# Optimization experiments

Hardware: AMD Instinct MI355X
Metric: run time of the kernel (lower is better)

## Reference

```python
import jax, jax.numpy as jnp
import numpy as np

# Layer configuration (from init_kwargs)
T = 32
TSEQ = jnp.linspace(1.0 / T, 1.0, T, dtype=jnp.float32)  # tseq grid
N_HOM_DIMS = 2      # dimensions = [0, 1]
KMAX = 4            # KK = [0,1,2,3] -> top-4 landscapes

B, N, P = 128, 256 * 256, 4096  # batch, grid cells, persistence pairs


def setup_inputs() -> dict:
    key = jax.random.key(0)
    k1, k2, k3, k4 = jax.random.split(key, 4)
    fun_value = jax.random.uniform(k1, (B, N), dtype=jnp.float32)
    birth_idx = jax.random.randint(k2, (B, P), 0, N, dtype=jnp.int32)
    death_idx = jax.random.randint(k3, (B, P), 0, N, dtype=jnp.int32)
    pair_dim = jax.random.randint(k4, (B, P), 0, N_HOM_DIMS, dtype=jnp.int32)
    return {"fun_value": fun_value, "birth_idx": birth_idx,
            "death_idx": death_idx, "pair_dim": pair_dim}


def reference(fun_value, birth_idx, death_idx, pair_dim):
    # Gather birth/death filtration values of each persistence pair
    # (this is fun_value[locationBirth] / fun_value[locationDeath]).
    b = jnp.take_along_axis(fun_value, birth_idx, axis=-1)   # [B, P]
    d = jnp.take_along_axis(fun_value, death_idx, axis=-1)   # [B, P]
    # Tent functions: fab[b, t, p] = max(min(tseq[t] - birth_p, death_p - tseq[t]), 0)
    fab = jnp.maximum(
        jnp.minimum(TSEQ[None, :, None] - b[:, None, :],
                    d[:, None, :] - TSEQ[None, :, None]),
        0.0)                                                  # [B, T, P]
    # Restrict pairs to each homology dimension; out-of-dim pairs become the
    # zero padding the original code uses in its fab buffer.
    dims = jnp.arange(N_HOM_DIMS, dtype=pair_dim.dtype)
    in_dim = pair_dim[:, None, None, :] == dims[None, :, None, None]  # [B, D, 1, P]
    fab_d = jnp.where(in_dim, fab[:, None, :, :], 0.0)        # [B, D, T, P]
    # Landscape = top-KMAX values over pairs (== -sort(-fab)[..., KK]).
    land, _ = jax.lax.top_k(fab_d, KMAX)                      # [B, D, T, KMAX]
    return land
```

## Files before the change

### kernel.cpp

```cpp
#include <hip/hip_runtime.h>

#define B_ 128
#define N_ 65536
#define P_ 4096
#define T_ 32
#define D_ 2
#define K_ 4
#define S_ 8
#define PAIRS_PER_BLOCK (P_ / S_)
#define PAIRS_PER_WAVE (PAIRS_PER_BLOCK / 4)

__global__ __launch_bounds__(256) void gather_bd(
        const float* __restrict__ fun,
        const int* __restrict__ bidx,
        const int* __restrict__ didx,
        float2* __restrict__ bd) {
    int tid = blockIdx.x * 256 + threadIdx.x;
    int batch = tid >> 12;
    const float* f = fun + (size_t)batch * N_;
    float b = f[bidx[tid]];
    float d = f[didx[tid]];
    bd[tid] = make_float2(b, d);
}

__global__ __launch_bounds__(256) void scan_top4(
        const float2* __restrict__ bd,
        const int* __restrict__ pdim,
        float* __restrict__ partial) {
    __shared__ float2 bdS[PAIRS_PER_BLOCK];
    __shared__ int    pdS[PAIRS_PER_BLOCK];
    __shared__ float  mrg[4][64][4];

    int batch = blockIdx.x;
    int slice = blockIdx.y;
    int tid   = threadIdx.x;
    int base  = batch * P_ + slice * PAIRS_PER_BLOCK;

    for (int i = tid; i < PAIRS_PER_BLOCK; i += 256) {
        bdS[i] = bd[base + i];
        pdS[i] = pdim[base + i];
    }
    __syncthreads();

    int lane  = tid & 63;
    int wave  = tid >> 6;
    int t     = lane & 31;
    int mydim = lane >> 5;
    float tf  = (float)(t + 1) * 0.03125f;

    float v0 = 0.f, v1 = 0.f, v2 = 0.f, v3 = 0.f;
    int p0 = wave * PAIRS_PER_WAVE;
    #pragma unroll 4
    for (int i = 0; i < PAIRS_PER_WAVE; ++i) {
        float2 bdv = bdS[p0 + i];
        int   pd   = pdS[p0 + i];
        float tv   = fminf(tf - bdv.x, bdv.y - tf);
        float val  = (pd == mydim) ? tv : 0.0f;
        val = fmaxf(val, 0.0f);
        float x;
        x = fminf(v0, val); v0 = fmaxf(v0, val); val = x;
        x = fminf(v1, val); v1 = fmaxf(v1, val); val = x;
        x = fminf(v2, val); v2 = fmaxf(v2, val); val = x;
        v3 = fmaxf(v3, val);
    }

    mrg[wave][lane][0] = v0;
    mrg[wave][lane][1] = v1;
    mrg[wave][lane][2] = v2;
    mrg[wave][lane][3] = v3;
    __syncthreads();

    if (wave == 0) {
        float u0 = 0.f, u1 = 0.f, u2 = 0.f, u3 = 0.f;
        #pragma unroll
        for (int w = 0; w < 4; ++w) {
            #pragma unroll
            for (int k = 0; k < 4; ++k) {
                float val = mrg[w][lane][k];
                float x;
                x = fminf(u0, val); u0 = fmaxf(u0, val); val = x;
                x = fminf(u1, val); u1 = fmaxf(u1, val); val = x;
                x = fminf(u2, val); u2 = fmaxf(u2, val); val = x;
                u3 = fmaxf(u3, val);
            }
        }
        float* dst = partial + (((size_t)batch * S_ + slice) * 64 + lane) * 4;
        dst[0] = u0; dst[1] = u1; dst[2] = u2; dst[3] = u3;
    }
}

__global__ __launch_bounds__(256) void final_merge(
        const float* __restrict__ partial,
        float* __restrict__ out) {
    int tid = blockIdx.x * 256 + threadIdx.x;
    int batch = tid >> 6;
    int combo = tid & 63;
    float u0 = 0.f, u1 = 0.f, u2 = 0.f, u3 = 0.f;
    for (int s = 0; s < S_; ++s) {
        const float* src = partial + (((size_t)batch * S_ + s) * 64 + combo) * 4;
        #pragma unroll
        for (int k = 0; k < 4; ++k) {
            float val = src[k];
            float x;
            x = fminf(u0, val); u0 = fmaxf(u0, val); val = x;
            x = fminf(u1, val); u1 = fmaxf(u1, val); val = x;
            x = fminf(u2, val); u2 = fmaxf(u2, val); val = x;
            u3 = fmaxf(u3, val);
        }
    }
    float* dst = out + (size_t)tid * 4;
    dst[0] = u0; dst[1] = u1; dst[2] = u2; dst[3] = u3;
}

extern "C" void kernel_launch(void* const* d_in, const int* in_sizes, int n_in,
                              void* d_out, int out_size, void* d_ws, size_t ws_size,
                              hipStream_t stream) {
    const float* fun  = (const float*)d_in[0];
    const int*   bidx = (const int*)d_in[1];
    const int*   didx = (const int*)d_in[2];
    const int*   pdim = (const int*)d_in[3];
    float* out = (float*)d_out;

    float2* bdw     = (float2*)d_ws;
    float*  partial = (float*)d_ws + (size_t)B_ * P_ * 2;

    gather_bd<<<(B_ * P_) / 256, 256, 0, stream>>>(fun, bidx, didx, bdw);

    dim3 g2(B_, S_);
    scan_top4<<<g2, 256, 0, stream>>>(bdw, pdim, partial);

    final_merge<<<(B_ * 64) / 256, 256, 0, stream>>>(partial, out);
}
```

Before: 107.4 us.

## Fuse gather into scan, partition pairs by dimension, remap blocks per XCD

Merges the gather and scan kernels so each block reads its filtration values directly into shared memory, with no round trip through a workspace buffer. Within the block, pairs are split by homology dimension using ballot and prefix counts. Each half-wave then handles every pair of one dimension, rather than masking out half of all pairs. Block indices are remapped so that each XCD handles a contiguous group of batches, which should improve L2 locality of the gathered rows. The cost is extra ballot and prefix-sum overhead and uneven loop lengths between waves.

```diff
diff --git a/kernel.cpp b/kernel.cpp
--- a/kernel.cpp
+++ b/kernel.cpp
@@ -7,109 +7,143 @@
 #define D_ 2
 #define K_ 4
 #define S_ 8
-#define PAIRS_PER_BLOCK (P_ / S_)
-#define PAIRS_PER_WAVE (PAIRS_PER_BLOCK / 4)
+#define PPB 512
 
-__global__ __launch_bounds__(256) void gather_bd(
+#define INS(v0, v1, v2, v3, val)                                  \
+    {                                                             \
+        float _x = fminf(v0, val); v0 = fmaxf(v0, val);           \
+        float _y = fminf(v1, _x);  v1 = fmaxf(v1, _x);            \
+        float _z = fminf(v2, _y);  v2 = fmaxf(v2, _y);            \
+        v3 = fmaxf(v3, _z);                                       \
+    }
+
+__global__ __launch_bounds__(256) void fused_scan(
         const float* __restrict__ fun,
         const int* __restrict__ bidx,
         const int* __restrict__ didx,
-        float2* __restrict__ bd) {
-    int tid = blockIdx.x * 256 + threadIdx.x;
-    int batch = tid >> 12;
-    const float* f = fun + (size_t)batch * N_;
-    float b = f[bidx[tid]];
-    float d = f[didx[tid]];
-    bd[tid] = make_float2(b, d);
-}
-
-__global__ __launch_bounds__(256) void scan_top4(
-        const float2* __restrict__ bd,
         const int* __restrict__ pdim,
         float* __restrict__ partial) {
-    __shared__ float2 bdS[PAIRS_PER_BLOCK];
-    __shared__ int    pdS[PAIRS_PER_BLOCK];
+    __shared__ float2 bdS[PPB + 8];
+    __shared__ int    cntS[8];
     __shared__ float  mrg[4][64][4];
 
-    int batch = blockIdx.x;
-    int slice = blockIdx.y;
-    int tid   = threadIdx.x;
-    int base  = batch * P_ + slice * PAIRS_PER_BLOCK;
+    int bid   = blockIdx.x;
+    int xcd   = bid & 7;
+    int seq   = bid >> 3;
+    int batch = xcd * 16 + (seq & 15);
+    int slice = seq >> 4;
 
-    for (int i = tid; i < PAIRS_PER_BLOCK; i += 256) {
-        bdS[i] = bd[base + i];
-        pdS[i] = pdim[base + i];
+    int tid  = threadIdx.x;
+    int lane = tid & 63;
+    int wave = tid >> 6;
+    int base = batch * P_ + slice * PPB;
+
+    const float* f = fun + (size_t)batch * N_;
+    int p0 = base + tid, p1 = base + 256 + tid;
+    int pd0 = pdim[p0], pd1 = pdim[p1];
+    float b0 = f[bidx[p0]], d0 = f[didx[p0]];
+    float b1 = f[bidx[p1]], d1 = f[didx[p1]];
+
+    unsigned long long bal0 = __ballot(pd0 == 0);
+    unsigned long long bal1 = __ballot(pd1 == 0);
+    if (lane == 0) {
+        cntS[wave * 2]     = __popcll(bal0);
+        cntS[wave * 2 + 1] = __popcll(bal1);
     }
     __syncthreads();
 
-    int lane  = tid & 63;
-    int wave  = tid >> 6;
-    int t     = lane & 31;
-    int mydim = lane >> 5;
-    float tf  = (float)(t + 1) * 0.03125f;
+    int s0 = wave * 2, s1 = s0 + 1;
+    int pre0_s0 = 0, pre1_s0 = 0, pre0_s1 = 0, pre1_s1 = 0, n0tot = 0;
+    #pragma unroll
+    for (int s = 0; s < 8; ++s) {
+        int cs = cntS[s];
+        if (s < s0) { pre0_s0 += cs; pre1_s0 += 64 - cs; }
+        if (s < s1) { pre0_s1 += cs; pre1_s1 += 64 - cs; }
+        n0tot += cs;
+    }
+    int n1tot = PPB - n0tot;
+    int A   = (n0tot + 1) & ~1;
+    int n1p = (n1tot + 1) & ~1;
 
-    float v0 = 0.f, v1 = 0.f, v2 = 0.f, v3 = 0.f;
-    int p0 = wave * PAIRS_PER_WAVE;
+    unsigned long long lmask = (1ull << lane) - 1ull;
+    int r0 = __popcll(bal0 & lmask);
+    int r1 = __popcll(bal1 & lmask);
+    int dst0 = (pd0 == 0) ? (pre0_s0 + r0) : (A + pre1_s0 + (lane - r0));
+    int dst1 = (pd1 == 0) ? (pre0_s1 + r1) : (A + pre1_s1 + (lane - r1));
+    bdS[dst0] = make_float2(b0, d0);
+    bdS[dst1] = make_float2(b1, d1);
+    if (tid == 0 && (n0tot & 1)) bdS[n0tot]     = make_float2(4.f, -4.f);
+    if (tid == 1 && (n1tot & 1)) bdS[A + n1tot] = make_float2(4.f, -4.f);
+    __syncthreads();
+
+    int half = lane >> 5;
+    int t    = lane & 31;
+    float tf = (float)(t + 1) * 0.03125f;
+
+    float a0 = 0.f, a1 = 0.f, a2 = 0.f, a3 = 0.f;
+    float c0 = 0.f, c1 = 0.f, c2 = 0.f, c3 = 0.f;
+
     #pragma unroll 4
-    for (int i = 0; i < PAIRS_PER_WAVE; ++i) {
-        float2 bdv = bdS[p0 + i];
-        int   pd   = pdS[p0 + i];
-        float tv   = fminf(tf - bdv.x, bdv.y - tf);
-        float val  = (pd == mydim) ? tv : 0.0f;
-        val = fmaxf(val, 0.0f);
-        float x;
-        x = fminf(v0, val); v0 = fmaxf(v0, val); val = x;
-        x = fminf(v1, val); v1 = fmaxf(v1, val); val = x;
-        x = fminf(v2, val); v2 = fmaxf(v2, val); val = x;
-        v3 = fmaxf(v3, val);
+    for (int j = wave * 2; j < A; j += 8) {
+        float2 p = bdS[j + half];
+        float val = fminf(tf - p.x, p.y - tf);
+        INS(a0, a1, a2, a3, val);
+    }
+    #pragma unroll 4
+    for (int j = A + wave * 2; j < A + n1p; j += 8) {
+        float2 p = bdS[j + half];
+        float val = fminf(tf - p.x, p.y - tf);
+        INS(c0, c1, c2, c3, val);
     }
 
-    mrg[wave][lane][0] = v0;
-    mrg[wave][lane][1] = v1;
-    mrg[wave][lane][2] = v2;
-    mrg[wave][lane][3] = v3;
+    float u0 = (half == 0) ? a0 : c0, w0 = (half == 0) ? c0 : a0;
+    float u1 = (half == 0) ? a1 : c1, w1 = (half == 0) ? c1 : a1;
+    float u2 = (half == 0) ? a2 : c2, w2 = (half == 0) ? c2 : a2;
+    float u3 = (half == 0) ? a3 : c3, w3 = (half == 0) ? c3 : a3;
+    float q;
+    q = __shfl_xor(w0, 32); INS(u0, u1, u2, u3, q);
+    q = __shfl_xor(w1, 32); INS(u0, u1, u2, u3, q);
+    q = __shfl_xor(w2, 32); INS(u0, u1, u2, u3, q);
+    q = __shfl_xor(w3, 32); INS(u0, u1, u2, u3, q);
+
+    mrg[wave][lane][0] = u0;
+    mrg[wave][lane][1] = u1;
+    mrg[wave][lane][2] = u2;
+    mrg[wave][lane][3] = u3;
     __syncthreads();
 
     if (wave == 0) {
-        float u0 = 0.f, u1 = 0.f, u2 = 0.f, u3 = 0.f;
+        float v0 = 0.f, v1 = 0.f, v2 = 0.f, v3 = 0.f;
         #pragma unroll
         for (int w = 0; w < 4; ++w) {
             #pragma unroll
             for (int k = 0; k < 4; ++k) {
                 float val = mrg[w][lane][k];
-                float x;
-                x = fminf(u0, val); u0 = fmaxf(u0, val); val = x;
-                x = fminf(u1, val); u1 = fmaxf(u1, val); val = x;
-                x = fminf(u2, val); u2 = fmaxf(u2, val); val = x;
-                u3 = fmaxf(u3, val);
+                INS(v0, v1, v2, v3, val);
             }
         }
         float* dst = partial + (((size_t)batch * S_ + slice) * 64 + lane) * 4;
-        dst[0] = u0; dst[1] = u1; dst[2] = u2; dst[3] = u3;
+        dst[0] = v0; dst[1] = v1; dst[2] = v2; dst[3] = v3;
     }
 }
 
 __global__ __launch_bounds__(256) void final_merge(
         const float* __restrict__ partial,
         float* __restrict__ out) {
-    int tid = blockIdx.x * 256 + threadIdx.x;
+    int tid   = blockIdx.x * 256 + threadIdx.x;
     int batch = tid >> 6;
     int combo = tid & 63;
-    float u0 = 0.f, u1 = 0.f, u2 = 0.f, u3 = 0.f;
+    float v0 = 0.f, v1 = 0.f, v2 = 0.f, v3 = 0.f;
     for (int s = 0; s < S_; ++s) {
         const float* src = partial + (((size_t)batch * S_ + s) * 64 + combo) * 4;
         #pragma unroll
         for (int k = 0; k < 4; ++k) {
             float val = src[k];
-            float x;
-            x = fminf(u0, val); u0 = fmaxf(u0, val); val = x;
-            x = fminf(u1, val); u1 = fmaxf(u1, val); val = x;
-            x = fminf(u2, val); u2 = fmaxf(u2, val); val = x;
-            u3 = fmaxf(u3, val);
+            INS(v0, v1, v2, v3, val);
         }
     }
     float* dst = out + (size_t)tid * 4;
-    dst[0] = u0; dst[1] = u1; dst[2] = u2; dst[3] = u3;
+    dst[0] = v0; dst[1] = v1; dst[2] = v2; dst[3] = v3;
 }
 
 extern "C" void kernel_launch(void* const* d_in, const int* in_sizes, int n_in,
@@ -121,13 +155,8 @@
     const int*   pdim = (const int*)d_in[3];
     float* out = (float*)d_out;
 
-    float2* bdw     = (float2*)d_ws;
-    float*  partial = (float*)d_ws + (size_t)B_ * P_ * 2;
+    float* partial = (float*)d_ws;
 
-    gather_bd<<<(B_ * P_) / 256, 256, 0, stream>>>(fun, bidx, didx, bdw);
-
-    dim3 g2(B_, S_);
-    scan_top4<<<g2, 256, 0, stream>>>(bdw, pdim, partial);
-
+    fused_scan<<<B_ * S_, 256, 0, stream>>>(fun, bidx, didx, pdim, partial);
     final_merge<<<(B_ * 64) / 256, 256, 0, stream>>>(partial, out);
 }
```

Measured after the change: 89.61 us. 1.2x faster.
